# Kernel optimization log

Hardware: AMD Instinct MI355X
Metric: run time of the kernel (lower is better)

Reference implementation:

```python
import jax, jax.numpy as jnp
import numpy as np

TEMPERATURE = 0.01
VMIN, VMAX = -1.0, 1.0
NUM_VALUES = 256


def setup_inputs() -> dict:
    key = jax.random.key(0)
    k_img, k_cmap = jax.random.split(key)
    image = jax.random.uniform(k_img, (4, 3, 512, 512), dtype=jnp.float32)
    cmap = jax.random.uniform(k_cmap, (NUM_VALUES, 3), dtype=jnp.float32)
    idx = jnp.arange(NUM_VALUES, dtype=jnp.float32)
    v_i = VMIN + (VMAX - VMIN) * idx / (NUM_VALUES - 1)
    return {"image": image, "cmap": cmap, "v_i": v_i}


def reference(image, cmap, v_i):
    # image: (N, 3, H, W) -> (N, H, W, 3)
    img = jnp.transpose(image, (0, 2, 3, 1))
    # squared euclidean distance to each of the 256 colormap colors
    # dist[n,h,w,k] = sum_c (img[n,h,w,c] - cmap[k,c])^2
    diff = img[..., None, :] - cmap  # (N, H, W, K, 3)
    distances = jnp.sum(diff * diff, axis=-1)  # (N, H, W, K)
    weights = jax.nn.softmax(-distances / TEMPERATURE, axis=-1)
    velocities = jnp.einsum('nhwk,k->nhw', weights, v_i)
    return velocities
```

## Files before the change

### kernel.cpp

```cpp
#include <hip/hip_runtime.h>


typedef __attribute__((ext_vector_type(8))) short short8;
typedef __attribute__((ext_vector_type(4))) float f32x4;
typedef __attribute__((ext_vector_type(2))) float v2f;

#define HWSZ 262144
#define NPIX 1048576
#define K2F  144.2695040888963f

static __device__ __forceinline__ unsigned f2bf(float x, float* resid) {
  unsigned u = __builtin_bit_cast(unsigned, x);
  unsigned r = (u + 0x7fffu + ((u >> 16) & 1u)) >> 16;
  if (resid) *resid = x - __builtin_bit_cast(float, r << 16);
  return r;
}
static __device__ __forceinline__ unsigned bfp(unsigned lo, unsigned hi) {
  return (lo & 0xffffu) | (hi << 16);
}

__global__ __launch_bounds__(256) void rgb2vel_prep(
    const float* __restrict__ cmap, float4* __restrict__ btab) {
  int k = threadIdx.x;
  float c0 = cmap[k * 3 + 0], c1 = cmap[k * 3 + 1], c2 = cmap[k * 3 + 2];
  float cc[3] = {c0, c1, c2};
  unsigned H[3], M[3], L[3];
  float r;
#pragma unroll
  for (int ch = 0; ch < 3; ++ch) {
    float x = 2.0f * K2F * cc[ch];
    H[ch] = f2bf(x, &r);
    M[ch] = f2bf(r, &r);
    L[ch] = f2bf(r, nullptr);
  }
  float mcc = -(K2F * (c0 * c0 + c1 * c1 + c2 * c2));
  unsigned mh = f2bf(mcc, &r);
  unsigned mm = f2bf(r, &r);
  unsigned ml = f2bf(r, nullptr);
  const unsigned N1 = 0xBF80u;
  unsigned d[16];
  d[0] = bfp(H[0], H[1]); d[1] = bfp(H[2], H[0]); d[2] = bfp(H[1], H[2]);
  d[3] = bfp(M[0], M[1]); d[4] = bfp(M[2], L[0]); d[5] = bfp(L[1], L[2]);
  d[6] = bfp(M[0], M[1]); d[7] = bfp(M[2], H[0]); d[8] = bfp(H[1], H[2]);
  d[9] = bfp(mh, mm);     d[10] = bfp(ml, N1);    d[11] = bfp(N1, N1);
  d[12] = d[13] = d[14] = d[15] = 0u;
  int col = k & 15, tt = k >> 4;
#pragma unroll
  for (int g = 0; g < 4; ++g) {
    float4 v;
    v.x = __builtin_bit_cast(float, d[4 * g + 0]);
    v.y = __builtin_bit_cast(float, d[4 * g + 1]);
    v.z = __builtin_bit_cast(float, d[4 * g + 2]);
    v.w = __builtin_bit_cast(float, d[4 * g + 3]);
    btab[tt * 64 + g * 16 + col] = v;
  }
}

__global__ __launch_bounds__(512, 6) void rgb2vel_main(
    const float* __restrict__ img, const float4* __restrict__ btab,
    const float* __restrict__ vv, float* __restrict__ out) {
  __shared__ __align__(16) unsigned char sA[128 * 80];
  __shared__ __align__(16) float4 sB[1024];
  const int tid = threadIdx.x;
  const int lane = tid & 63;
  const int warp = tid >> 6;
  const int col = lane & 15;
  const int g = lane >> 4;
  const int pb0 = blockIdx.x * 128;

  sB[tid] = btab[tid];
  sB[tid + 512] = btab[tid + 512];

  if (tid < 128) {
    int idx = pb0 + tid;
    int n = idx >> 18;
    int hw = idx & (HWSZ - 1);
    const float* pb = img + (size_t)n * 3 * HWSZ + hw;
    float p0 = pb[0], p1 = pb[HWSZ], p2 = pb[2 * HWSZ];
    float pc[3] = {p0, p1, p2};
    unsigned ph[3], pm[3], pl[3];
    float r;
#pragma unroll
    for (int ch = 0; ch < 3; ++ch) {
      ph[ch] = f2bf(pc[ch], &r);
      pm[ch] = f2bf(r, &r);
      pl[ch] = f2bf(r, nullptr);
    }
    float q = K2F * (p0 * p0 + p1 * p1 + p2 * p2);
    unsigned qh = f2bf(q, &r);
    unsigned qm = f2bf(r, &r);
    unsigned ql = f2bf(r, nullptr);
    const unsigned ONE = 0x3F80u;
    int4* sb = (int4*)(sA + tid * 80);
    sb[0] = make_int4((int)bfp(ph[0], ph[1]), (int)bfp(ph[2], pm[0]),
                      (int)bfp(pm[1], pm[2]), (int)bfp(ph[0], ph[1]));
    sb[1] = make_int4((int)bfp(ph[2], ph[0]), (int)bfp(ph[1], ph[2]),
                      (int)bfp(pm[0], pm[1]), (int)bfp(pm[2], pl[0]));
    sb[2] = make_int4((int)bfp(pl[1], pl[2]), (int)bfp(ONE, ONE),
                      (int)bfp(ONE, qh),      (int)bfp(qm, ql));
    sb[3] = make_int4(0, 0, 0, 0);
  }

  float vk[16];
#pragma unroll
  for (int t = 0; t < 16; ++t) vk[t] = vv[t * 16 + col];

  __syncthreads();

  short8 afr = *(const short8*)(sA + (warp * 16 + col) * 80 + g * 16);

  v2f acc0 = {0.f, 0.f}, acc1 = {0.f, 0.f}, acc2 = {0.f, 0.f}, acc3 = {0.f, 0.f};
  const f32x4 z = {0.f, 0.f, 0.f, 0.f};

#pragma unroll
  for (int t = 0; t < 16; ++t) {
    short8 bfr = __builtin_bit_cast(short8, sB[t * 64 + lane]);
    f32x4 c = __builtin_amdgcn_mfma_f32_16x16x32_bf16(afr, bfr, z, 0, 0, 0);
    v2f cf = {1.0f, vk[t]};
    float w0 = __builtin_amdgcn_exp2f(c[0]);
    float w1 = __builtin_amdgcn_exp2f(c[1]);
    float w2 = __builtin_amdgcn_exp2f(c[2]);
    float w3 = __builtin_amdgcn_exp2f(c[3]);
    acc0 = __builtin_elementwise_fma((v2f){w0, w0}, cf, acc0);
    acc1 = __builtin_elementwise_fma((v2f){w1, w1}, cf, acc1);
    acc2 = __builtin_elementwise_fma((v2f){w2, w2}, cf, acc2);
    acc3 = __builtin_elementwise_fma((v2f){w3, w3}, cf, acc3);
  }

#pragma unroll
  for (int m = 1; m <= 8; m <<= 1) {
    acc0.x += __shfl_xor(acc0.x, m); acc0.y += __shfl_xor(acc0.y, m);
    acc1.x += __shfl_xor(acc1.x, m); acc1.y += __shfl_xor(acc1.y, m);
    acc2.x += __shfl_xor(acc2.x, m); acc2.y += __shfl_xor(acc2.y, m);
    acc3.x += __shfl_xor(acc3.x, m); acc3.y += __shfl_xor(acc3.y, m);
  }
  if (col < 4) {
    v2f a = (col == 0) ? acc0 : (col == 1) ? acc1 : (col == 2) ? acc2 : acc3;
    out[pb0 + warp * 16 + g * 4 + col] = a.y / a.x;
  }
}

extern "C" void kernel_launch(void* const* d_in, const int* in_sizes, int n_in,
                              void* d_out, int out_size, void* d_ws, size_t ws_size,
                              hipStream_t stream) {
  const float* image = (const float*)d_in[0];
  const float* cmap  = (const float*)d_in[1];
  const float* v_i   = (const float*)d_in[2];
  float* out = (float*)d_out;

  float4* btab = (float4*)d_ws;

  rgb2vel_prep<<<1, 256, 0, stream>>>(cmap, btab);
  rgb2vel_main<<<NPIX / 128, 512, 0, stream>>>(image, btab, v_i, out);
}
```

Measured before the change: 108.5 us.

## Fuse colormap prep into main kernel and reduce softmax weights via f16 MFMA

```diff
diff --git a/kernel.cpp b/kernel.cpp
--- a/kernel.cpp
+++ b/kernel.cpp
@@ -1,13 +1,15 @@
 #include <hip/hip_runtime.h>
+#include <hip/hip_fp16.h>
 
 
 typedef __attribute__((ext_vector_type(8))) short short8;
+typedef __attribute__((ext_vector_type(8))) _Float16 f16x8;
 typedef __attribute__((ext_vector_type(4))) float f32x4;
-typedef __attribute__((ext_vector_type(2))) float v2f;
 
 #define HWSZ 262144
 #define NPIX 1048576
 #define K2F  144.2695040888963f
+#define BIASF 14.0f
 
 static __device__ __forceinline__ unsigned f2bf(float x, float* resid) {
   unsigned u = __builtin_bit_cast(unsigned, x);
@@ -18,65 +20,83 @@
 static __device__ __forceinline__ unsigned bfp(unsigned lo, unsigned hi) {
   return (lo & 0xffffu) | (hi << 16);
 }
-
-__global__ __launch_bounds__(256) void rgb2vel_prep(
-    const float* __restrict__ cmap, float4* __restrict__ btab) {
-  int k = threadIdx.x;
-  float c0 = cmap[k * 3 + 0], c1 = cmap[k * 3 + 1], c2 = cmap[k * 3 + 2];
-  float cc[3] = {c0, c1, c2};
-  unsigned H[3], M[3], L[3];
-  float r;
-#pragma unroll
-  for (int ch = 0; ch < 3; ++ch) {
-    float x = 2.0f * K2F * cc[ch];
-    H[ch] = f2bf(x, &r);
-    M[ch] = f2bf(r, &r);
-    L[ch] = f2bf(r, nullptr);
-  }
-  float mcc = -(K2F * (c0 * c0 + c1 * c1 + c2 * c2));
-  unsigned mh = f2bf(mcc, &r);
-  unsigned mm = f2bf(r, &r);
-  unsigned ml = f2bf(r, nullptr);
-  const unsigned N1 = 0xBF80u;
-  unsigned d[16];
-  d[0] = bfp(H[0], H[1]); d[1] = bfp(H[2], H[0]); d[2] = bfp(H[1], H[2]);
-  d[3] = bfp(M[0], M[1]); d[4] = bfp(M[2], L[0]); d[5] = bfp(L[1], L[2]);
-  d[6] = bfp(M[0], M[1]); d[7] = bfp(M[2], H[0]); d[8] = bfp(H[1], H[2]);
-  d[9] = bfp(mh, mm);     d[10] = bfp(ml, N1);    d[11] = bfp(N1, N1);
-  d[12] = d[13] = d[14] = d[15] = 0u;
-  int col = k & 15, tt = k >> 4;
-#pragma unroll
-  for (int g = 0; g < 4; ++g) {
-    float4 v;
-    v.x = __builtin_bit_cast(float, d[4 * g + 0]);
-    v.y = __builtin_bit_cast(float, d[4 * g + 1]);
-    v.z = __builtin_bit_cast(float, d[4 * g + 2]);
-    v.w = __builtin_bit_cast(float, d[4 * g + 3]);
-    btab[tt * 64 + g * 16 + col] = v;
-  }
+static __device__ __forceinline__ unsigned pkrtz(float a, float b) {
+  return __builtin_bit_cast(unsigned, __builtin_amdgcn_cvt_pkrtz(a, b));
 }
 
-__global__ __launch_bounds__(512, 6) void rgb2vel_main(
-    const float* __restrict__ img, const float4* __restrict__ btab,
+__global__ __launch_bounds__(512, 8) void rgb2vel_main(
+    const float* __restrict__ img, const float* __restrict__ cmap,
     const float* __restrict__ vv, float* __restrict__ out) {
   __shared__ __align__(16) unsigned char sA[128 * 80];
-  __shared__ __align__(16) float4 sB[1024];
+  __shared__ __align__(16) int4 sB4[1024];
+  __shared__ __align__(16) int4 sBv4[512];
   const int tid = threadIdx.x;
   const int lane = tid & 63;
   const int warp = tid >> 6;
-  const int col = lane & 15;
+  const int c = lane & 15;
   const int g = lane >> 4;
   const int pb0 = blockIdx.x * 128;
 
-  sB[tid] = btab[tid];
-  sB[tid + 512] = btab[tid + 512];
+  if (tid < 256) {
+    int k = tid;
+    float c0 = cmap[k * 3 + 0], c1 = cmap[k * 3 + 1], c2 = cmap[k * 3 + 2];
+    float cc[3] = {c0, c1, c2};
+    unsigned H[3], M[3], L[3];
+    float r;
+#pragma unroll
+    for (int ch = 0; ch < 3; ++ch) {
+      float x = 2.0f * K2F * cc[ch];
+      H[ch] = f2bf(x, &r);
+      M[ch] = f2bf(r, &r);
+      L[ch] = f2bf(r, nullptr);
+    }
+    float mcc = BIASF - K2F * (c0 * c0 + c1 * c1 + c2 * c2);
+    unsigned mh = f2bf(mcc, &r);
+    unsigned mm = f2bf(r, &r);
+    unsigned ml = f2bf(r, nullptr);
+    const unsigned N1 = 0xBF80u;
+    unsigned d[16];
+    d[0] = bfp(H[0], H[1]); d[1] = bfp(H[2], H[0]); d[2] = bfp(H[1], H[2]);
+    d[3] = bfp(M[0], M[1]); d[4] = bfp(M[2], L[0]); d[5] = bfp(L[1], L[2]);
+    d[6] = bfp(M[0], M[1]); d[7] = bfp(M[2], H[0]); d[8] = bfp(H[1], H[2]);
+    d[9] = bfp(mh, mm);     d[10] = bfp(ml, N1);    d[11] = bfp(N1, N1);
+    d[12] = d[13] = d[14] = d[15] = 0u;
+    int col = k & 15, tt = k >> 4;
+#pragma unroll
+    for (int g2 = 0; g2 < 4; ++g2)
+      sB4[tt * 64 + g2 * 16 + col] =
+          make_int4((int)d[4 * g2 + 0], (int)d[4 * g2 + 1],
+                    (int)d[4 * g2 + 2], (int)d[4 * g2 + 3]);
+  }
 
-  if (tid < 128) {
-    int idx = pb0 + tid;
+  {
+    int u = tid >> 6, l = tid & 63, cc2 = l & 15, gg = l >> 4;
+    int4 q = make_int4(0, 0, 0, 0);
+    if (cc2 == 0) {
+      q = make_int4(0x3C003C00, 0x3C003C00, 0x3C003C00, 0x3C003C00);
+    } else if (cc2 == 1) {
+      unsigned hq[4];
+#pragma unroll
+      for (int jp = 0; jp < 4; ++jp) {
+        int j0 = 2 * jp, j1 = 2 * jp + 1;
+        int i0 = (2 * u + (j0 >> 2)) * 16 + gg * 4 + (j0 & 3);
+        int i1 = (2 * u + (j1 >> 2)) * 16 + gg * 4 + (j1 & 3);
+        unsigned h0 = (unsigned)__half_as_ushort(__float2half(vv[i0]));
+        unsigned h1 = (unsigned)__half_as_ushort(__float2half(vv[i1]));
+        hq[jp] = h0 | (h1 << 16);
+      }
+      q = make_int4((int)hq[0], (int)hq[1], (int)hq[2], (int)hq[3]);
+    }
+    sBv4[tid] = q;
+  }
+
+  if (tid >= 384) {
+    int px = tid & 127;
+    int idx = pb0 + px;
     int n = idx >> 18;
     int hw = idx & (HWSZ - 1);
-    const float* pb = img + (size_t)n * 3 * HWSZ + hw;
-    float p0 = pb[0], p1 = pb[HWSZ], p2 = pb[2 * HWSZ];
+    const float* pbp = img + (size_t)n * 3 * HWSZ + hw;
+    float p0 = pbp[0], p1 = pbp[HWSZ], p2 = pbp[2 * HWSZ];
     float pc[3] = {p0, p1, p2};
     unsigned ph[3], pm[3], pl[3];
     float r;
@@ -86,12 +106,12 @@
       pm[ch] = f2bf(r, &r);
       pl[ch] = f2bf(r, nullptr);
     }
-    float q = K2F * (p0 * p0 + p1 * p1 + p2 * p2);
-    unsigned qh = f2bf(q, &r);
+    float qv = K2F * (p0 * p0 + p1 * p1 + p2 * p2);
+    unsigned qh = f2bf(qv, &r);
     unsigned qm = f2bf(r, &r);
     unsigned ql = f2bf(r, nullptr);
     const unsigned ONE = 0x3F80u;
-    int4* sb = (int4*)(sA + tid * 80);
+    int4* sb = (int4*)(sA + px * 80);
     sb[0] = make_int4((int)bfp(ph[0], ph[1]), (int)bfp(ph[2], pm[0]),
                       (int)bfp(pm[1], pm[2]), (int)bfp(ph[0], ph[1]));
     sb[1] = make_int4((int)bfp(ph[2], ph[0]), (int)bfp(ph[1], ph[2]),
@@ -100,43 +120,38 @@
                       (int)bfp(ONE, qh),      (int)bfp(qm, ql));
     sb[3] = make_int4(0, 0, 0, 0);
   }
-
-  float vk[16];
-#pragma unroll
-  for (int t = 0; t < 16; ++t) vk[t] = vv[t * 16 + col];
-
   __syncthreads();
 
-  short8 afr = *(const short8*)(sA + (warp * 16 + col) * 80 + g * 16);
+  short8 pfr = *(const short8*)(sA + (warp * 16 + c) * 80 + g * 16);
 
-  v2f acc0 = {0.f, 0.f}, acc1 = {0.f, 0.f}, acc2 = {0.f, 0.f}, acc3 = {0.f, 0.f};
+  f32x4 acc = {0.f, 0.f, 0.f, 0.f};
   const f32x4 z = {0.f, 0.f, 0.f, 0.f};
 
 #pragma unroll
-  for (int t = 0; t < 16; ++t) {
-    short8 bfr = __builtin_bit_cast(short8, sB[t * 64 + lane]);
-    f32x4 c = __builtin_amdgcn_mfma_f32_16x16x32_bf16(afr, bfr, z, 0, 0, 0);
-    v2f cf = {1.0f, vk[t]};
-    float w0 = __builtin_amdgcn_exp2f(c[0]);
-    float w1 = __builtin_amdgcn_exp2f(c[1]);
-    float w2 = __builtin_amdgcn_exp2f(c[2]);
-    float w3 = __builtin_amdgcn_exp2f(c[3]);
-    acc0 = __builtin_elementwise_fma((v2f){w0, w0}, cf, acc0);
-    acc1 = __builtin_elementwise_fma((v2f){w1, w1}, cf, acc1);
-    acc2 = __builtin_elementwise_fma((v2f){w2, w2}, cf, acc2);
-    acc3 = __builtin_elementwise_fma((v2f){w3, w3}, cf, acc3);
+  for (int u = 0; u < 8; ++u) {
+    short8 ca = __builtin_bit_cast(short8, sB4[(2 * u) * 64 + lane]);
+    short8 cb = __builtin_bit_cast(short8, sB4[(2 * u + 1) * 64 + lane]);
+    f32x4 d0 = __builtin_amdgcn_mfma_f32_16x16x32_bf16(ca, pfr, z, 0, 0, 0);
+    f32x4 d1 = __builtin_amdgcn_mfma_f32_16x16x32_bf16(cb, pfr, z, 0, 0, 0);
+    union { unsigned w[4]; f16x8 v8; } wu;
+    wu.w[0] = pkrtz(__builtin_amdgcn_exp2f(d0[0]), __builtin_amdgcn_exp2f(d0[1]));
+    wu.w[1] = pkrtz(__builtin_amdgcn_exp2f(d0[2]), __builtin_amdgcn_exp2f(d0[3]));
+    wu.w[2] = pkrtz(__builtin_amdgcn_exp2f(d1[0]), __builtin_amdgcn_exp2f(d1[1]));
+    wu.w[3] = pkrtz(__builtin_amdgcn_exp2f(d1[2]), __builtin_amdgcn_exp2f(d1[3]));
+    f16x8 bv = __builtin_bit_cast(f16x8, sBv4[u * 64 + lane]);
+    acc = __builtin_amdgcn_mfma_f32_16x16x32_f16(wu.v8, bv, acc, 0, 0, 0);
   }
 
-#pragma unroll
-  for (int m = 1; m <= 8; m <<= 1) {
-    acc0.x += __shfl_xor(acc0.x, m); acc0.y += __shfl_xor(acc0.y, m);
-    acc1.x += __shfl_xor(acc1.x, m); acc1.y += __shfl_xor(acc1.y, m);
-    acc2.x += __shfl_xor(acc2.x, m); acc2.y += __shfl_xor(acc2.y, m);
-    acc3.x += __shfl_xor(acc3.x, m); acc3.y += __shfl_xor(acc3.y, m);
-  }
-  if (col < 4) {
-    v2f a = (col == 0) ? acc0 : (col == 1) ? acc1 : (col == 2) ? acc2 : acc3;
-    out[pb0 + warp * 16 + g * 4 + col] = a.y / a.x;
+  float p0 = __shfl_xor(acc[0], 1);
+  float p1 = __shfl_xor(acc[1], 1);
+  float p2 = __shfl_xor(acc[2], 1);
+  float p3 = __shfl_xor(acc[3], 1);
+  if (c == 0) {
+    float* o = out + pb0 + warp * 16 + g * 4;
+    o[0] = p0 / acc[0];
+    o[1] = p1 / acc[1];
+    o[2] = p2 / acc[2];
+    o[3] = p3 / acc[3];
   }
 }
 
@@ -148,8 +163,5 @@
   const float* v_i   = (const float*)d_in[2];
   float* out = (float*)d_out;
 
-  float4* btab = (float4*)d_ws;
-
-  rgb2vel_prep<<<1, 256, 0, stream>>>(cmap, btab);
-  rgb2vel_main<<<NPIX / 128, 512, 0, stream>>>(image, btab, v_i, out);
+  rgb2vel_main<<<NPIX / 128, 512, 0, stream>>>(image, cmap, v_i, out);
 }
```

Measured after the change: 100.6 us. 1.08x faster.
